# Kernel optimization log

Hardware: AMD Instinct MI355X
Metric: run time of the kernel (lower is better)

## Reference

```python
import jax, jax.numpy as jnp
import numpy as np

B, S, D = 4, 2048, 512
H, HD, RL = 8, 64, 64   # nheads, head_dim = D//H, rl_dim
TEMPER = 1.0
BETA = 1.0
SLOPE = 0.01  # LeakyReLU negative slope
LN_EPS = 1e-5


def setup_inputs() -> dict:
    key = jax.random.key(0)
    ks = jax.random.split(key, 12)
    scale = 0.02
    return {
        "h":   jax.random.normal(ks[0], (B, S, D), dtype=jnp.float32),
        "rh":  jax.random.normal(ks[1], (B, S, RL), dtype=jnp.float32),
        "Wl":  jax.random.normal(ks[2], (D, D), dtype=jnp.float32) * scale,   # linear_l (in,out)
        "Wr":  jax.random.normal(ks[3], (D, D), dtype=jnp.float32) * scale,   # linear_r
        "al":  jax.random.normal(ks[4], (HD,), dtype=jnp.float32) * scale,    # att_l: Linear(head_dim,1)
        "ar":  jax.random.normal(ks[5], (HD,), dtype=jnp.float32) * scale,    # att_r
        "Wrs": jax.random.normal(ks[6], (RL, RL * H), dtype=jnp.float32) * scale,  # r_source
        "Wrt": jax.random.normal(ks[7], (RL, RL * H), dtype=jnp.float32) * scale,  # r_target
        "Wf":  jax.random.normal(ks[8], (D, D), dtype=jnp.float32) * scale,   # linear_final
        "ln_g": jnp.ones((D,), dtype=jnp.float32),
        "ln_b": jnp.zeros((D,), dtype=jnp.float32),
    }


def _layer_norm(x, g, b):
    mu = jnp.mean(x, axis=-1, keepdims=True)
    var = jnp.mean(jnp.square(x - mu), axis=-1, keepdims=True)
    return (x - mu) * jax.lax.rsqrt(var + LN_EPS) * g + b


def reference(h, rh, Wl, Wr, al, ar, Wrs, Wrt, Wf, ln_g, ln_b):
    leaky = lambda x: jnp.where(x >= 0, x, SLOPE * x)
    # projections -> [B, H, S, HD]
    fl = (h @ Wl).reshape(B, S, H, HD).transpose(0, 2, 1, 3)
    fr = (h @ Wr).reshape(B, S, H, HD).transpose(0, 2, 1, 3)
    # additive attention logits: [B,H,S,1] + [B,H,1,S]
    sl = jnp.einsum('bhsd,d->bhs', leaky(fl), al)
    sr = jnp.einsum('bhsd,d->bhs', leaky(fr), ar)
    score = sl[:, :, :, None] + sr[:, :, None, :]
    # relation-embedding bilinear bias: r_k @ r_q -> [B,H,S,S]
    r_k = (rh @ Wrs).reshape(B, S, H, RL).transpose(0, 2, 1, 3)   # [B,H,S,RL]
    r_q = (rh @ Wrt).reshape(B, S, H, RL).transpose(0, 2, 3, 1)   # [B,H,RL,S]
    score = score + BETA * jnp.einsum('bhsr,bhrt->bhst', r_k, r_q)
    score = jax.nn.softmax(score / TEMPER, axis=-1)
    # context and output projection (dropout = 0 -> identity)
    context = jnp.einsum('bhst,bhtd->bhsd', score, fr)
    h_sa = context.transpose(0, 2, 1, 3).reshape(B, S, H * HD)
    fh = h_sa @ Wf
    return _layer_norm(h + fh, ln_g, ln_b)
```

## Files before the change

### kernel.cpp

```cpp
#include <hip/hip_runtime.h>
#include <math.h>

#define B_ 4
#define S_ 2048
#define D_ 512
#define H_ 8
#define HD_ 64
#define RL_ 64
#define LN_EPS 1e-5f
#define SLOPE 0.01f
#define LOG2E 1.4426950408889634f

typedef __attribute__((ext_vector_type(8))) __bf16 bf16x8;
typedef __attribute__((ext_vector_type(4))) float f32x4;

__device__ __forceinline__ float leaky(float x) { return x >= 0.f ? x : SLOPE * x; }

__device__ __forceinline__ ushort f2bf(float f) {
    union { float f; unsigned u; } v; v.f = f;
    unsigned r = v.u + 0x7fffu + ((v.u >> 16) & 1u);
    return (ushort)(r >> 16);
}
__device__ __forceinline__ unsigned fbits(float f) {
    union { float f; unsigned u; } v; v.f = f; return v.u;
}

__device__ __forceinline__ void g2lds16(const void* g, void* l) {
    __builtin_amdgcn_global_load_lds(
        (const __attribute__((address_space(1))) void*)(uintptr_t)g,
        (__attribute__((address_space(3))) void*)(uintptr_t)l, 16, 0, 0);
}

__global__ __launch_bounds__(256) void prep(
    const float* __restrict__ h, const float* __restrict__ rh,
    const float* __restrict__ Wr, const float* __restrict__ Wf,
    const float* __restrict__ Wrs, const float* __restrict__ Wrt,
    ushort* __restrict__ hb, ushort* __restrict__ rhb,
    ushort* __restrict__ WrT, ushort* __restrict__ WfT,
    ushort* __restrict__ WrsT, ushort* __restrict__ WrtT)
{
    const int bx = blockIdx.x, tid = threadIdx.x;
    if (bx < 4608) {
        const float* in = (bx < 4096) ? h : rh;
        ushort* o = (bx < 4096) ? hb : rhb;
        const int i = (bx < 4096 ? bx : bx - 4096) * 256 + tid;
        const float4 v = ((const float4*)in)[i];
        ushort4 u; u.x = f2bf(v.x); u.y = f2bf(v.y); u.z = f2bf(v.z); u.w = f2bf(v.w);
        ((ushort4*)o)[i] = u;
        return;
    }
    __shared__ float TS[64][65];
    int t = bx - 4608;
    const float* in; ushort* out; int K, tk, tn;
    if (t < 64)       { in = Wr;  out = WrT;  K = 512; tk = t & 7; tn = t >> 3; }
    else if (t < 128) { in = Wf;  out = WfT;  K = 512; t -= 64; tk = t & 7; tn = t >> 3; }
    else if (t < 136) { in = Wrs; out = WrsT; K = 64;  tk = 0; tn = t - 128; }
    else              { in = Wrt; out = WrtT; K = 64;  tk = 0; tn = t - 136; }
    const int k0 = tk * 64, n0 = tn * 64;
    const int r = tid >> 4, c4 = (tid & 15) * 4;
    #pragma unroll
    for (int p = 0; p < 4; ++p) {
        const int row = r + 16 * p;
        const float4 v = *(const float4*)(in + (size_t)(k0 + row) * 512 + n0 + c4);
        TS[row][c4] = v.x; TS[row][c4 + 1] = v.y;
        TS[row][c4 + 2] = v.z; TS[row][c4 + 3] = v.w;
    }
    __syncthreads();
    #pragma unroll
    for (int p = 0; p < 4; ++p) {
        const int nn = r + 16 * p;
        ushort4 o;
        o.x = f2bf(TS[c4 + 0][nn]); o.y = f2bf(TS[c4 + 1][nn]);
        o.z = f2bf(TS[c4 + 2][nn]); o.w = f2bf(TS[c4 + 3][nn]);
        *(ushort4*)(out + (size_t)(n0 + nn) * K + k0 + c4) = o;
    }
}

__global__ __launch_bounds__(256) void proj(
    const ushort* __restrict__ hb, const ushort* __restrict__ rhb,
    const ushort* __restrict__ WrT, const ushort* __restrict__ WrsT,
    const ushort* __restrict__ WrtT,
    ushort* __restrict__ frT, ushort* __restrict__ rkw, ushort* __restrict__ rqw,
    float* __restrict__ sred, const float* __restrict__ ar)
{
    __shared__ ushort As[2][64 * 32];
    __shared__ ushort Bs[2][128 * 32];

    const int tid = threadIdx.x;
    const int lane = tid & 63, w = tid >> 6;
    const int ln = lane & 15, quad = lane >> 4;
    const int wm = w >> 1, wn = w & 1;
    const int m0 = blockIdx.x * 64, n0 = blockIdx.y * 128;
    const int z = blockIdx.z;

    const ushort* A; const ushort* wt; ushort* co; float scl; int K;
    if (z == 0)      { A = hb;  wt = WrT;  co = frT; scl = LOG2E; K = 512; }
    else if (z == 1) { A = rhb; wt = WrsT; co = rkw; scl = LOG2E; K = 64; }
    else             { A = rhb; wt = WrtT; co = rqw; scl = 1.0f;  K = 64; }

    const int srA = tid >> 2;
    const int lchA = ((lane & 3) - (srA >> 1)) & 3;
    const ushort* AgB = A + (size_t)(m0 + srA) * K + lchA * 8;
    const int srB = w * 32 + (lane >> 2);
    const int lchB = ((lane & 3) - (srB >> 1)) & 3;
    const ushort* BgB0 = wt + (size_t)(n0 + srB) * K + lchB * 8;
    const ushort* BgB1 = BgB0 + (size_t)16 * K;
    const int aoff = tid * 8;
    const int boff = srB * 32 + (lane & 3) * 8;
    const int pc = (quad + (ln >> 1)) & 3;

    g2lds16(AgB, &As[0][aoff]);
    g2lds16(BgB0, &Bs[0][boff]);
    g2lds16(BgB1, &Bs[0][boff + 512]);

    f32x4 acc[2][4] = {};
    int buf = 0;
    for (int k0 = 0; k0 < K; k0 += 32) {
        __syncthreads();
        if (k0 + 32 < K) {
            g2lds16(AgB + k0 + 32, &As[buf ^ 1][aoff]);
            g2lds16(BgB0 + k0 + 32, &Bs[buf ^ 1][boff]);
            g2lds16(BgB1 + k0 + 32, &Bs[buf ^ 1][boff + 512]);
        }
        bf16x8 af[2], bfr[4];
        #pragma unroll
        for (int mi = 0; mi < 2; ++mi)
            af[mi] = *(const bf16x8*)&As[buf][(wm * 32 + mi * 16 + ln) * 32 + pc * 8];
        #pragma unroll
        for (int ni = 0; ni < 4; ++ni)
            bfr[ni] = *(const bf16x8*)&Bs[buf][(wn * 64 + ni * 16 + ln) * 32 + pc * 8];
        #pragma unroll
        for (int mi = 0; mi < 2; ++mi)
            #pragma unroll
            for (int ni = 0; ni < 4; ++ni)
                acc[mi][ni] = __builtin_amdgcn_mfma_f32_16x16x32_bf16(
                    af[mi], bfr[ni], acc[mi][ni], 0, 0, 0);
        buf ^= 1;
    }

    const int head = blockIdx.y * 2 + wn;
    const int b = m0 >> 11;
    const size_t bh = (size_t)b * H_ + head;
    if (z == 0) {
        #pragma unroll
        for (int mi = 0; mi < 2; ++mi) {
            const int s = (m0 & (S_ - 1)) + wm * 32 + mi * 16 + quad * 4;
            #pragma unroll
            for (int ni = 0; ni < 4; ++ni) {
                const int d = ni * 16 + ln;
                ushort4 o;
                o.x = f2bf(acc[mi][ni][0]); o.y = f2bf(acc[mi][ni][1]);
                o.z = f2bf(acc[mi][ni][2]); o.w = f2bf(acc[mi][ni][3]);
                *(ushort4*)(co + (bh * 64 + d) * S_ + s) = o;
            }
        }
        float a4[4];
        #pragma unroll
        for (int ni = 0; ni < 4; ++ni) a4[ni] = ar[ni * 16 + ln];
        #pragma unroll
        for (int mi = 0; mi < 2; ++mi) {
            const int s = (m0 & (S_ - 1)) + wm * 32 + mi * 16 + quad * 4;
            #pragma unroll
            for (int r = 0; r < 4; ++r) {
                float v = 0.f;
                #pragma unroll
                for (int ni = 0; ni < 4; ++ni)
                    v += leaky(acc[mi][ni][r]) * a4[ni];
                #pragma unroll
                for (int off = 8; off; off >>= 1) v += __shfl_xor(v, off, 16);
                if (ln == 0) sred[bh * S_ + s + r] = v * scl;
            }
        }
    } else {
        #pragma unroll
        for (int mi = 0; mi < 2; ++mi) {
            const int s = (m0 & (S_ - 1)) + wm * 32 + mi * 16 + quad * 4;
            #pragma unroll
            for (int ni = 0; ni < 4; ++ni) {
                const int d = ni * 16 + ln;
                #pragma unroll
                for (int r = 0; r < 4; ++r)
                    co[(bh * S_ + s + r) * 64 + d] = f2bf(acc[mi][ni][r] * scl);
            }
        }
    }
}

#define WAITV(N) asm volatile("s_waitcnt vmcnt(" #N ")" ::: "memory")
#define BARR()   __builtin_amdgcn_s_barrier()

__global__ __launch_bounds__(256, 2) void attn_mfma(
    const ushort* __restrict__ frT, const ushort* __restrict__ rk,
    const ushort* __restrict__ rq, const float* __restrict__ sr,
    ushort* __restrict__ hsa)
{
    __shared__ ushort RQ[4][64][64];
    __shared__ ushort FT[4][64][64];
    __shared__ ushort PS[8][16][64];

    const int tid = threadIdx.x;
    const int w = tid >> 6;
    const int lane = tid & 63;
    const int ln = lane & 15;
    const int quad = lane >> 4;

    const int flat = blockIdx.x + 16 * (blockIdx.y + 8 * blockIdx.z);
    const int wid = (flat & 7) * 64 + (flat >> 3);
    const int q0 = (wid & 15) * 128;
    const int h = (wid >> 4) & 7;
    const int b = wid >> 7;
    const size_t bh = (size_t)b * H_ + h;

    bf16x8 a[2][2];
    #pragma unroll
    for (int qs = 0; qs < 2; ++qs) {
        const ushort* p = rk + ((bh * S_ + q0 + 32 * w + 16 * qs + ln) << 6);
        a[qs][0] = *(const bf16x8*)(p + quad * 8);
        a[qs][1] = *(const bf16x8*)(p + 32 + quad * 8);
    }

    const ushort* rq_g = rq + (bh * S_ << 6);
    const ushort* ft_g = frT + (size_t)bh * 64 * S_;
    const float* srp = sr + bh * S_;

    const int rl = lane >> 3;
    const int pg = lane & 7;
    const int row_b = w * 16 + rl;
    const int sgF = (pg - rl) & 7;
    const int sgR0 = (pg - 4 * w - (rl >> 2)) & 7;
    const int sgR1 = (pg - 4 * w - 2 - (rl >> 2)) & 7;

    #define STAGE(BUF, t0)                                                    \
        {                                                                     \
            g2lds16(rq_g + ((size_t)((t0) + row_b) << 6) + sgR0 * 8,          \
                    &RQ[BUF][row_b][pg * 8]);                                 \
            g2lds16(rq_g + ((size_t)((t0) + row_b + 8) << 6) + sgR1 * 8,      \
                    &RQ[BUF][row_b + 8][pg * 8]);                             \
            g2lds16(ft_g + (size_t)row_b * S_ + (t0) + sgF * 8,               \
                    &FT[BUF][row_b][pg * 8]);                                 \
            g2lds16(ft_g + (size_t)(row_b + 8) * S_ + (t0) + sgF * 8,         \
                    &FT[BUF][row_b + 8][pg * 8]);                             \
        }

    const ushort* rqrA = &RQ[0][0][0] + 4 * ln * 64 + ((quad + ln) & 7) * 8;
    const ushort* rqrB = &RQ[0][0][0] + 4 * ln * 64 + ((quad + 4 + ln) & 7) * 8;
    const ushort* ftrA = &FT[0][0][0] + ln * 64 + ((quad + ln) & 7) * 8;
    const ushort* ftrB = &FT[0][0][0] + ln * 64 + ((quad + 4 + ln) & 7) * 8;
    ushort* sb[2];
    sb[0] = &PS[w * 2][0][0]; sb[1] = &PS[w * 2 + 1][0][0];
    int wr_off[4];
    #pragma unroll
    for (int r = 0; r < 4; ++r) {
        const int prow = quad * 4 + r;
        wr_off[r] = prow * 64 + (((ln >> 1) + prow) & 7) * 8 + (ln & 1) * 4;
    }
    const int rd0 = ln * 64 + ((quad + ln) & 7) * 8;
    const int rd1 = ln * 64 + ((quad + 4 + ln) & 7) * 8;

    float lsum[2][4] = {};
    f32x4 ctx[2][4] = {};

    #define COMPUTE(BI, SV)                                                        \
        {                                                                          \
            f32x4 sc[2][4];                                                        \
            _Pragma("unroll")                                                      \
            for (int jb = 0; jb < 4; ++jb) {                                       \
                const bf16x8 b0 = *(const bf16x8*)(rqrA + (BI) * 4096 + jb * 64);  \
                const bf16x8 b1 = *(const bf16x8*)(rqrB + (BI) * 4096 + jb * 64);  \
                _Pragma("unroll")                                                  \
                for (int qs = 0; qs < 2; ++qs) {                                   \
                    f32x4 tt = {0.f, 0.f, 0.f, 0.f};                               \
                    tt = __builtin_amdgcn_mfma_f32_16x16x32_bf16(a[qs][0], b0, tt, 0, 0, 0); \
                    tt = __builtin_amdgcn_mfma_f32_16x16x32_bf16(a[qs][1], b1, tt, 0, 0, 0); \
                    sc[qs][jb] = tt;                                               \
                }                                                                  \
            }                                                                      \
            _Pragma("unroll")                                                      \
            for (int qs = 0; qs < 2; ++qs)                                         \
                _Pragma("unroll")                                                  \
                for (int r = 0; r < 4; ++r) {                                      \
                    const float p0 = __builtin_amdgcn_exp2f(sc[qs][0][r] + SV.x);  \
                    const float p1 = __builtin_amdgcn_exp2f(sc[qs][1][r] + SV.y);  \
                    const float p2 = __builtin_amdgcn_exp2f(sc[qs][2][r] + SV.z);  \
                    const float p3 = __builtin_amdgcn_exp2f(sc[qs][3][r] + SV.w);  \
                    lsum[qs][r] += (p0 + p1) + (p2 + p3);                          \
                    const unsigned lo = (fbits(p0) >> 16) | (fbits(p1) & 0xffff0000u); \
                    const unsigned hi = (fbits(p2) >> 16) | (fbits(p3) & 0xffff0000u); \
                    *(uint2*)(sb[qs] + wr_off[r]) = make_uint2(lo, hi);            \
                }                                                                  \
            const bf16x8 pa00 = *(const bf16x8*)(sb[0] + rd0);                     \
            const bf16x8 pa01 = *(const bf16x8*)(sb[0] + rd1);                     \
            const bf16x8 pa10 = *(const bf16x8*)(sb[1] + rd0);                     \
            const bf16x8 pa11 = *(const bf16x8*)(sb[1] + rd1);                     \
            _Pragma("unroll")                                                      \
            for (int jb = 0; jb < 4; ++jb) {                                       \
                const bf16x8 fb0 = *(const bf16x8*)(ftrA + (BI) * 4096 + jb * 1024); \
                const bf16x8 fb1 = *(const bf16x8*)(ftrB + (BI) * 4096 + jb * 1024); \
                ctx[0][jb] = __builtin_amdgcn_mfma_f32_16x16x32_bf16(pa00, fb0, ctx[0][jb], 0, 0, 0); \
                ctx[0][jb] = __builtin_amdgcn_mfma_f32_16x16x32_bf16(pa01, fb1, ctx[0][jb], 0, 0, 0); \
                ctx[1][jb] = __builtin_amdgcn_mfma_f32_16x16x32_bf16(pa10, fb0, ctx[1][jb], 0, 0, 0); \
                ctx[1][jb] = __builtin_amdgcn_mfma_f32_16x16x32_bf16(pa11, fb1, ctx[1][jb], 0, 0, 0); \
            }                                                                      \
        }

    float4 sv0, sv1, sv2, sv3;
    STAGE(0, 0)   sv0 = *(const float4*)(srp + 0 + 4 * ln);
    STAGE(1, 64)  sv1 = *(const float4*)(srp + 64 + 4 * ln);

    for (int it = 0; it < 7; ++it) {
        const int t0 = it * 256;
        WAITV(5); BARR();
        STAGE(2, t0 + 128) sv2 = *(const float4*)(srp + t0 + 128 + 4 * ln);
        COMPUTE(0, sv0)
        WAITV(5); BARR();
        STAGE(3, t0 + 192) sv3 = *(const float4*)(srp + t0 + 192 + 4 * ln);
        COMPUTE(1, sv1)
        WAITV(5); BARR();
        STAGE(0, t0 + 256) sv0 = *(const float4*)(srp + t0 + 256 + 4 * ln);
        COMPUTE(2, sv2)
        WAITV(5); BARR();
        STAGE(1, t0 + 320) sv1 = *(const float4*)(srp + t0 + 320 + 4 * ln);
        COMPUTE(3, sv3)
    }
    WAITV(5); BARR();
    STAGE(2, 1920) sv2 = *(const float4*)(srp + 1920 + 4 * ln);
    COMPUTE(0, sv0)
    WAITV(5); BARR();
    STAGE(3, 1984) sv3 = *(const float4*)(srp + 1984 + 4 * ln);
    COMPUTE(1, sv1)
    WAITV(5); BARR();
    COMPUTE(2, sv2)
    WAITV(0); BARR();
    COMPUTE(3, sv3)

    #pragma unroll
    for (int qs = 0; qs < 2; ++qs)
        #pragma unroll
        for (int r = 0; r < 4; ++r) {
            float l = lsum[qs][r];
            #pragma unroll
            for (int off = 8; off; off >>= 1) l += __shfl_xor(l, off, 16);
            const float inv = 1.f / l;
            const int q = q0 + 32 * w + 16 * qs + quad * 4 + r;
            ushort* orow = hsa + (size_t)(b * S_ + q) * D_ + h * 64;
            #pragma unroll
            for (int jb = 0; jb < 4; ++jb)
                orow[16 * jb + ln] = f2bf(ctx[qs][jb][r] * inv);
        }
}

__global__ __launch_bounds__(256) void gemm_out(
    const ushort* __restrict__ A, const ushort* __restrict__ WT,
    float* __restrict__ C)
{
    __shared__ ushort As[2][64 * 32];
    __shared__ ushort Bs[2][128 * 32];

    const int tid = threadIdx.x;
    const int lane = tid & 63, w = tid >> 6;
    const int ln = lane & 15, quad = lane >> 4;
    const int wm = w >> 1, wn = w & 1;
    const int m0 = blockIdx.x * 64, n0 = blockIdx.y * 128;
    const int K = 512;

    const int srA = tid >> 2;
    const int lchA = ((lane & 3) - (srA >> 1)) & 3;
    const ushort* AgB = A + (size_t)(m0 + srA) * K + lchA * 8;
    const int srB = w * 32 + (lane >> 2);
    const int lchB = ((lane & 3) - (srB >> 1)) & 3;
    const ushort* BgB0 = WT + (size_t)(n0 + srB) * K + lchB * 8;
    const ushort* BgB1 = BgB0 + (size_t)16 * K;
    const int aoff = tid * 8;
    const int boff = srB * 32 + (lane & 3) * 8;
    const int pc = (quad + (ln >> 1)) & 3;

    g2lds16(AgB, &As[0][aoff]);
    g2lds16(BgB0, &Bs[0][boff]);
    g2lds16(BgB1, &Bs[0][boff + 512]);

    f32x4 acc[2][4] = {};
    int buf = 0;
    for (int k0 = 0; k0 < K; k0 += 32) {
        __syncthreads();
        if (k0 + 32 < K) {
            g2lds16(AgB + k0 + 32, &As[buf ^ 1][aoff]);
            g2lds16(BgB0 + k0 + 32, &Bs[buf ^ 1][boff]);
            g2lds16(BgB1 + k0 + 32, &Bs[buf ^ 1][boff + 512]);
        }
        bf16x8 af[2], bfr[4];
        #pragma unroll
        for (int mi = 0; mi < 2; ++mi)
            af[mi] = *(const bf16x8*)&As[buf][(wm * 32 + mi * 16 + ln) * 32 + pc * 8];
        #pragma unroll
        for (int ni = 0; ni < 4; ++ni)
            bfr[ni] = *(const bf16x8*)&Bs[buf][(wn * 64 + ni * 16 + ln) * 32 + pc * 8];
        #pragma unroll
        for (int mi = 0; mi < 2; ++mi)
            #pragma unroll
            for (int ni = 0; ni < 4; ++ni)
                acc[mi][ni] = __builtin_amdgcn_mfma_f32_16x16x32_bf16(
                    af[mi], bfr[ni], acc[mi][ni], 0, 0, 0);
        buf ^= 1;
    }

    #pragma unroll
    for (int mi = 0; mi < 2; ++mi) {
        const int row = m0 + wm * 32 + mi * 16 + quad * 4;
        #pragma unroll
        for (int ni = 0; ni < 4; ++ni) {
            const int col = n0 + wn * 64 + ni * 16 + ln;
            #pragma unroll
            for (int r = 0; r < 4; ++r)
                C[(size_t)(row + r) * 512 + col] = acc[mi][ni][r];
        }
    }
}

__global__ __launch_bounds__(256) void ln_kernel(
    const float* __restrict__ h, const float* __restrict__ fh,
    const float* __restrict__ g, const float* __restrict__ bb,
    float* __restrict__ out)
{
    const int row = blockIdx.x, tid = threadIdx.x;
    const float* hp = h + (size_t)row * 512;
    const float* fp = fh + (size_t)row * 512;
    const float x0 = hp[tid] + fp[tid];
    const float x1 = hp[tid + 256] + fp[tid + 256];
    __shared__ float red[4];

    float s = x0 + x1;
    #pragma unroll
    for (int off = 32; off; off >>= 1) s += __shfl_xor(s, off, 64);
    if ((tid & 63) == 0) red[tid >> 6] = s;
    __syncthreads();
    const float mu = (red[0] + red[1] + red[2] + red[3]) * (1.f / 512.f);

    const float d0 = x0 - mu, d1 = x1 - mu;
    float v = d0 * d0 + d1 * d1;
    #pragma unroll
    for (int off = 32; off; off >>= 1) v += __shfl_xor(v, off, 64);
    __syncthreads();
    if ((tid & 63) == 0) red[tid >> 6] = v;
    __syncthreads();
    const float var = (red[0] + red[1] + red[2] + red[3]) * (1.f / 512.f);
    const float inv = rsqrtf(var + LN_EPS);

    out[(size_t)row * 512 + tid] = d0 * inv * g[tid] + bb[tid];
    out[(size_t)row * 512 + tid + 256] = d1 * inv * g[tid + 256] + bb[tid + 256];
}

extern "C" void kernel_launch(void* const* d_in, const int* in_sizes, int n_in,
                              void* d_out, int out_size, void* d_ws, size_t ws_size,
                              hipStream_t stream)
{
    const float* h   = (const float*)d_in[0];
    const float* rh  = (const float*)d_in[1];
    const float* Wr  = (const float*)d_in[3];
    const float* ar  = (const float*)d_in[5];
    const float* Wrs = (const float*)d_in[6];
    const float* Wrt = (const float*)d_in[7];
    const float* Wf  = (const float*)d_in[8];
    const float* lng = (const float*)d_in[9];
    const float* lnb = (const float*)d_in[10];
    float* out = (float*)d_out;
    char* wsb  = (char*)d_ws;

    const size_t MB = (size_t)1 << 20;
    ushort* hb   = (ushort*)(wsb);
    ushort* rhb  = (ushort*)(wsb + 8 * MB);
    ushort* WrT  = (ushort*)(wsb + 9 * MB);
    ushort* WfT  = (ushort*)(wsb + 9 * MB + 512 * 1024);
    ushort* WrsT = (ushort*)(wsb + 10 * MB);
    ushort* WrtT = (ushort*)(wsb + 10 * MB + 64 * 1024);
    ushort* frT  = (ushort*)(wsb + 11 * MB);
    ushort* rkw  = (ushort*)(wsb + 19 * MB);
    ushort* rqw  = (ushort*)(wsb + 27 * MB);
    float*  sr   = (float*) (wsb + 35 * MB);
    ushort* hsab = (ushort*)(wsb + 36 * MB);
    float*  fh   = (float*) (wsb + 44 * MB);

    dim3 blk(256);
    prep<<<dim3(4752), blk, 0, stream>>>(h, rh, Wr, Wf, Wrs, Wrt,
                                         hb, rhb, WrT, WfT, WrsT, WrtT);
    proj<<<dim3(128, 4, 3), blk, 0, stream>>>(hb, rhb, WrT, WrsT, WrtT,
                                              frT, rkw, rqw, sr, ar);
    attn_mfma<<<dim3(S_ / 128, H_, B_), blk, 0, stream>>>(frT, rkw, rqw, sr, hsab);
    gemm_out<<<dim3(128, 4), blk, 0, stream>>>(hsab, WfT, fh);
    ln_kernel<<<dim3(B_ * S_), blk, 0, stream>>>(h, fh, lng, lnb, out);
}
```

Measured before the change: 172.4 us.

## Software-pipeline attention loop: overlap next tile's QK^T MFMAs with current softmax/PV

Splits the per-tile compute into a score GEMM (QKT) and a softmax+PV stage (SMPV), then runs the score GEMM for tile i+1 before the softmax/PV of tile i, using two score register sets. This lets the MFMA work of one tile overlap the exp/pack/LDS work of the previous one. It also raises wave priority with s_setprio around the MFMA sections. In exchange it uses more VGPRs for the second score buffer, which may lower occupancy, and the buffer-index ordering across stages must stay correct.

Result: slower. 205.8 us (+19.4%).

```diff
diff --git a/kernel.cpp b/kernel.cpp
--- a/kernel.cpp
+++ b/kernel.cpp
@@ -259,79 +259,96 @@
 
     float lsum[2][4] = {};
     f32x4 ctx[2][4] = {};
-
-    #define COMPUTE(BI, SV)                                                        \
-        {                                                                          \
-            f32x4 sc[2][4];                                                        \
-            _Pragma("unroll")                                                      \
-            for (int jb = 0; jb < 4; ++jb) {                                       \
-                const bf16x8 b0 = *(const bf16x8*)(rqrA + (BI) * 4096 + jb * 64);  \
-                const bf16x8 b1 = *(const bf16x8*)(rqrB + (BI) * 4096 + jb * 64);  \
-                _Pragma("unroll")                                                  \
-                for (int qs = 0; qs < 2; ++qs) {                                   \
-                    f32x4 tt = {0.f, 0.f, 0.f, 0.f};                               \
+    f32x4 scA[2][4], scB[2][4];
+
+    #define QKT(BI, SC)                                                       \
+        {                                                                     \
+            __builtin_amdgcn_s_setprio(1);                                    \
+            _Pragma("unroll")                                                 \
+            for (int jb = 0; jb < 4; ++jb) {                                  \
+                const bf16x8 b0 = *(const bf16x8*)(rqrA + (BI) * 4096 + jb * 64); \
+                const bf16x8 b1 = *(const bf16x8*)(rqrB + (BI) * 4096 + jb * 64); \
+                _Pragma("unroll")                                             \
+                for (int qs = 0; qs < 2; ++qs) {                              \
+                    f32x4 tt = {0.f, 0.f, 0.f, 0.f};                          \
                     tt = __builtin_amdgcn_mfma_f32_16x16x32_bf16(a[qs][0], b0, tt, 0, 0, 0); \
                     tt = __builtin_amdgcn_mfma_f32_16x16x32_bf16(a[qs][1], b1, tt, 0, 0, 0); \
-                    sc[qs][jb] = tt;                                               \
-                }                                                                  \
-            }                                                                      \
-            _Pragma("unroll")                                                      \
-            for (int qs = 0; qs < 2; ++qs)                                         \
-                _Pragma("unroll")                                                  \
-                for (int r = 0; r < 4; ++r) {                                      \
-                    const float p0 = __builtin_amdgcn_exp2f(sc[qs][0][r] + SV.x);  \
-                    const float p1 = __builtin_amdgcn_exp2f(sc[qs][1][r] + SV.y);  \
-                    const float p2 = __builtin_amdgcn_exp2f(sc[qs][2][r] + SV.z);  \
-                    const float p3 = __builtin_amdgcn_exp2f(sc[qs][3][r] + SV.w);  \
-                    lsum[qs][r] += (p0 + p1) + (p2 + p3);                          \
+                    SC[qs][jb] = tt;                                          \
+                }                                                             \
+            }                                                                 \
+            __builtin_amdgcn_s_setprio(0);                                    \
+        }
+
+    #define SMPV(SC, SV, BJ)                                                  \
+        {                                                                     \
+            _Pragma("unroll")                                                 \
+            for (int qs = 0; qs < 2; ++qs)                                    \
+                _Pragma("unroll")                                             \
+                for (int r = 0; r < 4; ++r) {                                 \
+                    const float p0 = __builtin_amdgcn_exp2f(SC[qs][0][r] + SV.x); \
+                    const float p1 = __builtin_amdgcn_exp2f(SC[qs][1][r] + SV.y); \
+                    const float p2 = __builtin_amdgcn_exp2f(SC[qs][2][r] + SV.z); \
+                    const float p3 = __builtin_amdgcn_exp2f(SC[qs][3][r] + SV.w); \
+                    lsum[qs][r] += (p0 + p1) + (p2 + p3);                      \
                     const unsigned lo = (fbits(p0) >> 16) | (fbits(p1) & 0xffff0000u); \
                     const unsigned hi = (fbits(p2) >> 16) | (fbits(p3) & 0xffff0000u); \
-                    *(uint2*)(sb[qs] + wr_off[r]) = make_uint2(lo, hi);            \
-                }                                                                  \
-            const bf16x8 pa00 = *(const bf16x8*)(sb[0] + rd0);                     \
-            const bf16x8 pa01 = *(const bf16x8*)(sb[0] + rd1);                     \
-            const bf16x8 pa10 = *(const bf16x8*)(sb[1] + rd0);                     \
-            const bf16x8 pa11 = *(const bf16x8*)(sb[1] + rd1);                     \
-            _Pragma("unroll")                                                      \
-            for (int jb = 0; jb < 4; ++jb) {                                       \
-                const bf16x8 fb0 = *(const bf16x8*)(ftrA + (BI) * 4096 + jb * 1024); \
-                const bf16x8 fb1 = *(const bf16x8*)(ftrB + (BI) * 4096 + jb * 1024); \
+                    *(uint2*)(sb[qs] + wr_off[r]) = make_uint2(lo, hi);       \
+                }                                                             \
+            const bf16x8 pa00 = *(const bf16x8*)(sb[0] + rd0);                \
+            const bf16x8 pa01 = *(const bf16x8*)(sb[0] + rd1);                \
+            const bf16x8 pa10 = *(const bf16x8*)(sb[1] + rd0);                \
+            const bf16x8 pa11 = *(const bf16x8*)(sb[1] + rd1);                \
+            __builtin_amdgcn_s_setprio(1);                                    \
+            _Pragma("unroll")                                                 \
+            for (int jb = 0; jb < 4; ++jb) {                                  \
+                const bf16x8 fb0 = *(const bf16x8*)(ftrA + (BJ) * 4096 + jb * 1024); \
+                const bf16x8 fb1 = *(const bf16x8*)(ftrB + (BJ) * 4096 + jb * 1024); \
                 ctx[0][jb] = __builtin_amdgcn_mfma_f32_16x16x32_bf16(pa00, fb0, ctx[0][jb], 0, 0, 0); \
                 ctx[0][jb] = __builtin_amdgcn_mfma_f32_16x16x32_bf16(pa01, fb1, ctx[0][jb], 0, 0, 0); \
                 ctx[1][jb] = __builtin_amdgcn_mfma_f32_16x16x32_bf16(pa10, fb0, ctx[1][jb], 0, 0, 0); \
                 ctx[1][jb] = __builtin_amdgcn_mfma_f32_16x16x32_bf16(pa11, fb1, ctx[1][jb], 0, 0, 0); \
-            }                                                                      \
+            }                                                                 \
+            __builtin_amdgcn_s_setprio(0);                                    \
         }
 
     float4 sv0, sv1, sv2, sv3;
     STAGE(0, 0)   sv0 = *(const float4*)(srp + 0 + 4 * ln);
     STAGE(1, 64)  sv1 = *(const float4*)(srp + 64 + 4 * ln);
 
-    for (int it = 0; it < 7; ++it) {
-        const int t0 = it * 256;
-        WAITV(5); BARR();
-        STAGE(2, t0 + 128) sv2 = *(const float4*)(srp + t0 + 128 + 4 * ln);
-        COMPUTE(0, sv0)
-        WAITV(5); BARR();
-        STAGE(3, t0 + 192) sv3 = *(const float4*)(srp + t0 + 192 + 4 * ln);
-        COMPUTE(1, sv1)
+    WAITV(5); BARR();
+    STAGE(2, 128) sv2 = *(const float4*)(srp + 128 + 4 * ln);
+    QKT(0, scA)
+    WAITV(5); BARR();
+    STAGE(3, 192) sv3 = *(const float4*)(srp + 192 + 4 * ln);
+    QKT(1, scB)
+    SMPV(scA, sv0, 0)
+
+    for (int k = 0; k < 7; ++k) {
+        const int t0 = k * 256;
         WAITV(5); BARR();
         STAGE(0, t0 + 256) sv0 = *(const float4*)(srp + t0 + 256 + 4 * ln);
-        COMPUTE(2, sv2)
+        QKT(2, scA)
+        SMPV(scB, sv1, 1)
         WAITV(5); BARR();
         STAGE(1, t0 + 320) sv1 = *(const float4*)(srp + t0 + 320 + 4 * ln);
-        COMPUTE(3, sv3)
+        QKT(3, scB)
+        SMPV(scA, sv2, 2)
+        WAITV(5); BARR();
+        STAGE(2, t0 + 384) sv2 = *(const float4*)(srp + t0 + 384 + 4 * ln);
+        QKT(0, scA)
+        SMPV(scB, sv3, 3)
+        WAITV(5); BARR();
+        STAGE(3, t0 + 448) sv3 = *(const float4*)(srp + t0 + 448 + 4 * ln);
+        QKT(1, scB)
+        SMPV(scA, sv0, 0)
     }
     WAITV(5); BARR();
-    STAGE(2, 1920) sv2 = *(const float4*)(srp + 1920 + 4 * ln);
-    COMPUTE(0, sv0)
-    WAITV(5); BARR();
-    STAGE(3, 1984) sv3 = *(const float4*)(srp + 1984 + 4 * ln);
-    COMPUTE(1, sv1)
-    WAITV(5); BARR();
-    COMPUTE(2, sv2)
+    QKT(2, scA)
+    SMPV(scB, sv1, 1)
     WAITV(0); BARR();
-    COMPUTE(3, sv3)
+    QKT(3, scB)
+    SMPV(scA, sv2, 2)
+    SMPV(scB, sv3, 3)
 
     #pragma unroll
     for (int qs = 0; qs < 2; ++qs)
```

## Shrink attention blocks to 64 queries with 2 waves and double buffering

Applied to the files above, without the earlier changes.

The attention kernel now uses 128-thread blocks, each covering 64 query rows, so there are twice as many blocks (32x8x4). LDS staging drops from four buffers to two, with each wave loading 32 rows per stage, and the pipeline waits on vmcnt(0) before every barrier. This cuts LDS use per block, allowing more blocks per CU and finer-grained scheduling. In exchange there is less prefetch depth, since loads are no longer kept several stages ahead. K/V tiles are also reused across fewer queries, which doubles global traffic for RQ and FT.

New measurement: 176.7 us. 2.5% more time.

```diff
diff --git a/kernel.cpp b/kernel.cpp
--- a/kernel.cpp
+++ b/kernel.cpp
@@ -189,14 +189,14 @@
 #define WAITV(N) asm volatile("s_waitcnt vmcnt(" #N ")" ::: "memory")
 #define BARR()   __builtin_amdgcn_s_barrier()
 
-__global__ __launch_bounds__(256, 2) void attn_mfma(
+__global__ __launch_bounds__(128, 2) void attn_mfma(
     const ushort* __restrict__ frT, const ushort* __restrict__ rk,
     const ushort* __restrict__ rq, const float* __restrict__ sr,
     ushort* __restrict__ hsa)
 {
-    __shared__ ushort RQ[4][64][64];
-    __shared__ ushort FT[4][64][64];
-    __shared__ ushort PS[8][16][64];
+    __shared__ ushort RQ[2][64][64];
+    __shared__ ushort FT[2][64][64];
+    __shared__ ushort PS[4][16][64];
 
     const int tid = threadIdx.x;
     const int w = tid >> 6;
@@ -204,11 +204,11 @@
     const int ln = lane & 15;
     const int quad = lane >> 4;
 
-    const int flat = blockIdx.x + 16 * (blockIdx.y + 8 * blockIdx.z);
-    const int wid = (flat & 7) * 64 + (flat >> 3);
-    const int q0 = (wid & 15) * 128;
-    const int h = (wid >> 4) & 7;
-    const int b = wid >> 7;
+    const int flat = blockIdx.x + 32 * (blockIdx.y + 8 * blockIdx.z);
+    const int wid = (flat & 7) * 128 + (flat >> 3);
+    const int q0 = (wid & 31) * 64;
+    const int h = (wid >> 5) & 7;
+    const int b = wid >> 8;
     const size_t bh = (size_t)b * H_ + h;
 
     bf16x8 a[2][2];
@@ -225,21 +225,20 @@
 
     const int rl = lane >> 3;
     const int pg = lane & 7;
-    const int row_b = w * 16 + rl;
+    const int base_row = w * 32 + rl;
     const int sgF = (pg - rl) & 7;
-    const int sgR0 = (pg - 4 * w - (rl >> 2)) & 7;
-    const int sgR1 = (pg - 4 * w - 2 - (rl >> 2)) & 7;
 
     #define STAGE(BUF, t0)                                                    \
         {                                                                     \
-            g2lds16(rq_g + ((size_t)((t0) + row_b) << 6) + sgR0 * 8,          \
-                    &RQ[BUF][row_b][pg * 8]);                                 \
-            g2lds16(rq_g + ((size_t)((t0) + row_b + 8) << 6) + sgR1 * 8,      \
-                    &RQ[BUF][row_b + 8][pg * 8]);                             \
-            g2lds16(ft_g + (size_t)row_b * S_ + (t0) + sgF * 8,               \
-                    &FT[BUF][row_b][pg * 8]);                                 \
-            g2lds16(ft_g + (size_t)(row_b + 8) * S_ + (t0) + sgF * 8,         \
-                    &FT[BUF][row_b + 8][pg * 8]);                             \
+            _Pragma("unroll")                                                 \
+            for (int m = 0; m < 4; ++m) {                                     \
+                const int rr = base_row + 8 * m;                              \
+                const int sgR = (pg - ((rr >> 2) & 7)) & 7;                   \
+                g2lds16(rq_g + ((size_t)((t0) + rr) << 6) + sgR * 8,          \
+                        &RQ[BUF][rr][pg * 8]);                                \
+                g2lds16(ft_g + (size_t)rr * S_ + (t0) + sgF * 8,              \
+                        &FT[BUF][rr][pg * 8]);                                \
+            }                                                                 \
         }
 
     const ushort* rqrA = &RQ[0][0][0] + 4 * ln * 64 + ((quad + ln) & 7) * 8;
@@ -303,35 +302,23 @@
             }                                                                      \
         }
 
-    float4 sv0, sv1, sv2, sv3;
-    STAGE(0, 0)   sv0 = *(const float4*)(srp + 0 + 4 * ln);
-    STAGE(1, 64)  sv1 = *(const float4*)(srp + 64 + 4 * ln);
-
-    for (int it = 0; it < 7; ++it) {
-        const int t0 = it * 256;
-        WAITV(5); BARR();
-        STAGE(2, t0 + 128) sv2 = *(const float4*)(srp + t0 + 128 + 4 * ln);
+    float4 sv0, sv1;
+    STAGE(0, 0)  sv0 = *(const float4*)(srp + 0 + 4 * ln);
+
+    for (int it = 0; it < 15; ++it) {
+        const int t0 = it * 128;
+        WAITV(0); BARR();
+        STAGE(1, t0 + 64)   sv1 = *(const float4*)(srp + t0 + 64 + 4 * ln);
         COMPUTE(0, sv0)
-        WAITV(5); BARR();
-        STAGE(3, t0 + 192) sv3 = *(const float4*)(srp + t0 + 192 + 4 * ln);
+        WAITV(0); BARR();
+        STAGE(0, t0 + 128)  sv0 = *(const float4*)(srp + t0 + 128 + 4 * ln);
         COMPUTE(1, sv1)
-        WAITV(5); BARR();
-        STAGE(0, t0 + 256) sv0 = *(const float4*)(srp + t0 + 256 + 4 * ln);
-        COMPUTE(2, sv2)
-        WAITV(5); BARR();
-        STAGE(1, t0 + 320) sv1 = *(const float4*)(srp + t0 + 320 + 4 * ln);
-        COMPUTE(3, sv3)
-    }
-    WAITV(5); BARR();
-    STAGE(2, 1920) sv2 = *(const float4*)(srp + 1920 + 4 * ln);
+    }
+    WAITV(0); BARR();
+    STAGE(1, 1984)  sv1 = *(const float4*)(srp + 1984 + 4 * ln);
     COMPUTE(0, sv0)
-    WAITV(5); BARR();
-    STAGE(3, 1984) sv3 = *(const float4*)(srp + 1984 + 4 * ln);
+    WAITV(0); BARR();
     COMPUTE(1, sv1)
-    WAITV(5); BARR();
-    COMPUTE(2, sv2)
-    WAITV(0); BARR();
-    COMPUTE(3, sv3)
 
     #pragma unroll
     for (int qs = 0; qs < 2; ++qs)
@@ -484,7 +471,7 @@
                                          hb, rhb, WrT, WfT, WrsT, WrtT);
     proj<<<dim3(128, 4, 3), blk, 0, stream>>>(hb, rhb, WrT, WrsT, WrtT,
                                               frT, rkw, rqw, sr, ar);
-    attn_mfma<<<dim3(S_ / 128, H_, B_), blk, 0, stream>>>(frT, rkw, rqw, sr, hsab);
+    attn_mfma<<<dim3(S_ / 64, H_, B_), dim3(128), 0, stream>>>(frT, rkw, rqw, sr, hsab);
     gemm_out<<<dim3(128, 4), blk, 0, stream>>>(hsab, WfT, fh);
     ln_kernel<<<dim3(B_ * S_), blk, 0, stream>>>(h, fh, lng, lnb, out);
 }
```
